# Performance work log

Hardware: AMD Instinct MI355X
Metric: run time of the kernel (lower is better)

## Reference

```python
import jax, jax.numpy as jnp
import numpy as np

B, I, J, DIM, H, DH = 2, 2048, 2048, 512, 8, 64
INNER = H * DH  # 512
SCALE = DH ** -0.5


def setup_inputs() -> dict:
    key = jax.random.key(0)
    ks = jax.random.split(key, 10)
    w = lambda k, shp: jax.random.normal(k, shp, dtype=jnp.float32) * 0.02
    return {
        "x": jax.random.normal(ks[0], (B, I, DIM), dtype=jnp.float32),
        "context": jax.random.normal(ks[1], (B, J, DIM), dtype=jnp.float32),
        "w_qk": w(ks[2], (DIM, INNER)),
        "w_cqk": w(ks[3], (DIM, INNER)),
        "w_v": w(ks[4], (DIM, INNER)),
        "w_cv": w(ks[5], (DIM, INNER)),
        "w_out": w(ks[6], (INNER, DIM)),
        "b_out": jnp.zeros((DIM,), dtype=jnp.float32),
        "w_cout": w(ks[7], (INNER, DIM)),
        "b_cout": jnp.zeros((DIM,), dtype=jnp.float32),
    }


def _split_heads(t):
    # [b, n, h*d] -> [b, h, n, d]
    b, n, _ = t.shape
    return t.reshape(b, n, H, DH).transpose(0, 2, 1, 3)


def reference(x, context, w_qk, w_cqk, w_v, w_cv, w_out, b_out, w_cout, b_cout):
    # projections (no bias, matching nn.Linear(..., bias=False))
    qk = _split_heads(x @ w_qk)            # [b,h,i,d]
    cqk = _split_heads(context @ w_cqk)    # [b,h,j,d]
    v = _split_heads(x @ w_v)              # [b,h,i,d]
    cv = _split_heads(context @ w_cv)      # [b,h,j,d]

    sim = jnp.einsum('bhid,bhjd->bhij', qk, cqk) * SCALE  # [b,h,i,j]

    attn = jax.nn.softmax(sim, axis=-1)        # row softmax over j
    context_attn = jax.nn.softmax(sim, axis=-2)  # column softmax over i

    out = jnp.einsum('bhij,bhjd->bhid', attn, cv)           # [b,h,i,d]
    context_out = jnp.einsum('bhji,bhjd->bhid', context_attn, v)  # [b,h,j_out=i? -> per einsum: i indexes last of attn]

    # merge heads: [b,h,n,d] -> [b,n,h*d]
    merge = lambda t: t.transpose(0, 2, 1, 3).reshape(t.shape[0], t.shape[2], INNER)
    out = merge(out) @ w_out + b_out                    # [b,i,dim]
    context_out = merge(context_out) @ w_cout + b_cout  # [b,j,dim]
    return (out, context_out)
```

## Files before the change

### kernel.cpp

```cpp
#include <hip/hip_runtime.h>

#define DEVI __device__ __forceinline__

typedef __attribute__((ext_vector_type(8))) short short8;
typedef __attribute__((ext_vector_type(4))) float f32x4;

struct alignas(8) us4 { unsigned short a, b, c, d; };

DEVI unsigned short f2bf(float f) {
    unsigned int u = __float_as_uint(f);
    u += 0x7fffU + ((u >> 16) & 1U);
    return (unsigned short)(u >> 16);
}

DEVI f32x4 mfma16(short8 a, short8 b, f32x4 c) {
    return __builtin_amdgcn_mfma_f32_16x16x32_bf16(a, b, c, 0, 0, 0);
}

DEVI unsigned pk2(float lo, float hi) {
    unsigned r0 = __float_as_uint(lo) + 0x8000u;
    unsigned r1 = __float_as_uint(hi) + 0x8000u;
    return __builtin_amdgcn_perm(r1, r0, 0x07060302u);
}

DEVI short8 mk8(unsigned a, unsigned b, unsigned c, unsigned d) {
    union { unsigned u[4]; short8 s; } x;
    x.u[0] = a; x.u[1] = b; x.u[2] = c; x.u[3] = d;
    return x.s;
}

#define GLDS(gp, sp) __builtin_amdgcn_global_load_lds( \
    (const __attribute__((address_space(1))) void*)(gp), \
    (__attribute__((address_space(3))) void*)(sp), 16, 0, 0)

#define VMCNT(n) asm volatile("s_waitcnt vmcnt(" #n ")" ::: "memory")
#define LGKMCNT0 asm volatile("s_waitcnt lgkmcnt(0)" ::: "memory")
#define MEMFENCE asm volatile("" ::: "memory")

#define SQC 0.42466089f

__global__ __launch_bounds__(256) void prep_kernel(
    const float* w0, const float* w1, const float* w2, const float* w3,
    const float* w4, const float* w5, short* __restrict__ wT)
{
    const float* srcs[6] = {w0, w1, w2, w3, w4, w5};
    int wz = blockIdx.x >> 6, rem = blockIdx.x & 63;
    const float* src = srcs[wz];
    short* dst = wT + (size_t)wz * 262144;
    int k0 = (rem >> 3) * 64, n0 = (rem & 7) * 64;
    __shared__ float tile[64][65];
    int t = threadIdx.x;
    int r = t >> 2, c0 = (t & 3) * 16;
#pragma unroll
    for (int ii = 0; ii < 4; ++ii) {
        float4 v = *(const float4*)(src + (size_t)(k0 + r) * 512 + n0 + c0 + ii * 4);
        tile[r][c0 + ii * 4 + 0] = v.x;
        tile[r][c0 + ii * 4 + 1] = v.y;
        tile[r][c0 + ii * 4 + 2] = v.z;
        tile[r][c0 + ii * 4 + 3] = v.w;
    }
    __syncthreads();
#pragma unroll
    for (int ii = 0; ii < 4; ++ii) {
        us4 o;
        o.a = f2bf(tile[c0 + ii * 4 + 0][r]);
        o.b = f2bf(tile[c0 + ii * 4 + 1][r]);
        o.c = f2bf(tile[c0 + ii * 4 + 2][r]);
        o.d = f2bf(tile[c0 + ii * 4 + 3][r]);
        *(us4*)(dst + (size_t)(n0 + r) * 512 + k0 + c0 + ii * 4) = o;
    }
}

__global__ __launch_bounds__(256, 4) void proj_kernel(
    const float* __restrict__ x, const float* __restrict__ ctx,
    const short* __restrict__ wT,
    short* __restrict__ QK, short* __restrict__ CQK,
    short* __restrict__ VT, short* __restrict__ CVT)
{
    __shared__ __align__(16) char smem[24576];
    short (*wst)[4096] = (short (*)[4096])smem;
    float (*ctile)[69] = (float (*)[69])smem;

    int p = blockIdx.z;
    const float* src = (p & 1) ? ctx : x;
    const short* wm = wT + (size_t)p * 262144;
    int wid = threadIdx.x >> 6, lane = threadIdx.x & 63, il = lane & 15, q = lane >> 4;
    int mb = blockIdx.x * 64, nb = blockIdx.y * 64;
    int srow = lane >> 3, scol8 = ((lane & 7) ^ srow) << 3;
    int key = il & 7;
    const short* wL0 = wm + (size_t)(nb + wid * 16 + srow) * 512 + scol8;
    const short* wL1 = wL0 + 8 * 512;
#define PSTAGE(s, ck) do { \
    GLDS(wL0 + (ck) * 64, &wst[s][wid * 1024]); \
    GLDS(wL1 + (ck) * 64, &wst[s][wid * 1024 + 512]); } while (0)

    PSTAGE(0, 0);
    PSTAGE(1, 1);

    const float* arow = src + (size_t)(mb + wid * 16 + il) * 512;
    short8 a[16];
#pragma unroll
    for (int j = 0; j < 16; ++j) {
        float4 f0 = *(const float4*)(arow + j * 32 + q * 8);
        float4 f1 = *(const float4*)(arow + j * 32 + q * 8 + 4);
        a[j] = mk8(pk2(f0.x, f0.y), pk2(f0.z, f0.w),
                   pk2(f1.x, f1.y), pk2(f1.z, f1.w));
    }

    f32x4 acc[4] = {};
    int sA = 0, sB = 1, sC = 2;
    for (int ck = 0; ck < 8; ++ck) {
        if (ck < 7) { VMCNT(2); } else { VMCNT(0); }
        MEMFENCE;
        __builtin_amdgcn_s_barrier();
        if (ck < 6) PSTAGE(sC, ck + 2);
#pragma unroll
        for (int kk = 0; kk < 2; ++kk) {
#pragma unroll
            for (int nj = 0; nj < 4; ++nj) {
                short8 b = *(const short8*)(&wst[sA][(nj * 16 + il) * 64 + ((((kk << 2) + q) ^ key) << 3)]);
                acc[nj] = mfma16(a[ck * 2 + kk], b, acc[nj]);
            }
        }
        int t_ = sA; sA = sB; sB = sC; sC = t_;
    }
#undef PSTAGE

    __syncthreads();
#pragma unroll
    for (int nj = 0; nj < 4; ++nj)
#pragma unroll
        for (int r = 0; r < 4; ++r)
            ctile[wid * 16 + q * 4 + r][nj * 16 + il] = acc[nj][r];
    __syncthreads();
    int t = threadIdx.x, row = t >> 2, seg = (t & 3) << 4;
    short tmp[16];
    int h = blockIdx.y;
    if (p < 2) {
        short* dst = p ? CQK : QK;
        int i = mb + row, b2 = i >> 11, iL = i & 2047;
#pragma unroll
        for (int e = 0; e < 16; ++e) tmp[e] = (short)f2bf(ctile[row][seg + e] * SQC);
        short* dp = dst + (((size_t)b2 * 8 + h) * 2048 + iL) * 64 + seg;
        *(short8*)dp = *(const short8*)tmp;
        *(short8*)(dp + 8) = *(const short8*)(tmp + 8);
    } else {
        short* dst = (p == 2) ? VT : CVT;
        int d = row;
        int i0 = mb + seg, b2 = i0 >> 11, iL = i0 & 2047;
#pragma unroll
        for (int e = 0; e < 16; ++e) tmp[e] = (short)f2bf(ctile[seg + e][d]);
        short* dp = dst + (((size_t)b2 * 8 + h) * 64 + d) * 2048 + iL;
        *(short8*)dp = *(const short8*)tmp;
        *(short8*)(dp + 8) = *(const short8*)(tmp + 8);
    }
}

__global__ __launch_bounds__(256, 3) void attn_kernel(
    const short* __restrict__ QK, const short* __restrict__ CQK,
    const short* __restrict__ VT, const short* __restrict__ CVT,
    short* __restrict__ OUTx, short* __restrict__ OUTc)
{
    __shared__ __align__(16) short Bt[3][4096];
    __shared__ __align__(16) short Wt[3][4096];

    int flat = blockIdx.x + (blockIdx.y << 4) + (blockIdx.z << 8);
    int bh = flat & 15;
    int ib = (flat >> 4) & 15;
    int z = flat >> 8;

    const short* Arows = z ? CQK : QK;
    const short* Bcols = z ? QK : CQK;
    const short* WTm   = z ? VT : CVT;
    short* Om          = z ? OUTc : OUTx;

    int b_ = bh >> 3, h = bh & 7;
    int w = threadIdx.x >> 6, lane = threadIdx.x & 63, il = lane & 15, q = lane >> 4;
    const short* Ab = Arows + (size_t)bh * 131072;
    const short* Bb = Bcols + (size_t)bh * 131072;
    const short* Wb = WTm + (size_t)bh * 131072;

    int srow = lane >> 3;
    int scol8 = ((lane & 7) ^ srow) << 3;
    int key = il & 7;

    int p0 = w * 16 + srow, p1 = p0 + 8;
    int j0p = (p0 & 0x23) | ((p0 & 0x0C) << 1) | ((p0 & 0x10) >> 2);
    int j1p = (p1 & 0x23) | ((p1 & 0x0C) << 1) | ((p1 & 0x10) >> 2);
    const short* BbL0 = Bb + j0p * 64 + scol8;
    const short* BbL1 = Bb + j1p * 64 + scol8;
    const short* WbL0 = Wb + (size_t)p0 * 2048 + scol8;
    const short* WbL1 = WbL0 + 8 * 2048;

#define STAGE(s, jt) do { \
    GLDS(BbL0 + (jt) * 4096, &Bt[s][w * 1024]); \
    GLDS(BbL1 + (jt) * 4096, &Bt[s][w * 1024 + 512]); \
    GLDS(WbL0 + (jt) * 64, &Wt[s][w * 1024]); \
    GLDS(WbL1 + (jt) * 64, &Wt[s][w * 1024 + 512]); } while (0)

    short* Areg = (w < 2) ? &Bt[2][0] : &Wt[2][0];
    int ar = (w & 1) * 2048;
    {
        const short* AbL = Ab + (size_t)(ib * 128 + w * 32 + srow) * 64 + scol8;
        GLDS(AbL, Areg + ar);
        GLDS(AbL + 512, Areg + ar + 512);
        GLDS(AbL + 1024, Areg + ar + 1024);
        GLDS(AbL + 1536, Areg + ar + 1536);
    }
    STAGE(0, 0);
    STAGE(1, 1);
    VMCNT(8);

    short8 aq[2][2];
#pragma unroll
    for (int rg = 0; rg < 2; ++rg) {
        const short* base = Areg + ((w & 1) * 32 + rg * 16 + il) * 64;
        aq[rg][0] = *(const short8*)(base + ((q ^ key) << 3));
        aq[rg][1] = *(const short8*)(base + (((q + 4) ^ key) << 3));
    }
    LGKMCNT0;
    __builtin_amdgcn_sched_barrier(0);

    f32x4 acc[2][4] = {};
    float s_acc[2] = {0.f, 0.f};

    int sA = 0, sB = 1, sC = 2;
    for (int jt = 0; jt < 32; ++jt) {
        if (jt < 31) { VMCNT(4); } else { VMCNT(0); }
        MEMFENCE;
        __builtin_amdgcn_s_barrier();
        if (jt < 30) STAGE(sC, jt + 2);

        short8 b0[4], b1[4];
#pragma unroll
        for (int nj = 0; nj < 4; ++nj) {
            const short* bb = &Bt[sA][(nj * 16 + il) * 64];
            b0[nj] = *(const short8*)(bb + ((q ^ key) << 3));
            b1[nj] = *(const short8*)(bb + (((q + 4) ^ key) << 3));
        }

        unsigned pw[2][8];
#pragma unroll
        for (int rg = 0; rg < 2; ++rg) {
#pragma unroll
            for (int nj = 0; nj < 4; ++nj) {
                f32x4 zz = {};
                zz = mfma16(b0[nj], aq[rg][0], zz);
                zz = mfma16(b1[nj], aq[rg][1], zz);
                float e0 = __builtin_amdgcn_exp2f(zz[0]);
                float e1 = __builtin_amdgcn_exp2f(zz[1]);
                float e2 = __builtin_amdgcn_exp2f(zz[2]);
                float e3 = __builtin_amdgcn_exp2f(zz[3]);
                s_acc[rg] += (e0 + e1) + (e2 + e3);
                pw[rg][nj * 2 + 0] = pk2(e0, e1);
                pw[rg][nj * 2 + 1] = pk2(e2, e3);
            }
        }
        short8 pa0[2] = { mk8(pw[0][0], pw[0][1], pw[0][2], pw[0][3]),
                          mk8(pw[1][0], pw[1][1], pw[1][2], pw[1][3]) };
        short8 pa1[2] = { mk8(pw[0][4], pw[0][5], pw[0][6], pw[0][7]),
                          mk8(pw[1][4], pw[1][5], pw[1][6], pw[1][7]) };

#pragma unroll
        for (int nd = 0; nd < 4; ++nd) {
            const short* vv = &Wt[sA][(nd * 16 + il) * 64];
            short8 v0 = *(const short8*)(vv + ((q ^ key) << 3));
            short8 v1 = *(const short8*)(vv + (((q + 4) ^ key) << 3));
#pragma unroll
            for (int rg = 0; rg < 2; ++rg) {
                acc[rg][nd] = mfma16(pa0[rg], v0, acc[rg][nd]);
                acc[rg][nd] = mfma16(pa1[rg], v1, acc[rg][nd]);
            }
        }
        int t_ = sA; sA = sB; sB = sC; sC = t_;
    }
#undef STAGE

    f32x4 inv[2];
#pragma unroll
    for (int rg = 0; rg < 2; ++rg) {
        float s = s_acc[rg];
        s += __shfl_xor(s, 16);
        s += __shfl_xor(s, 32);
#pragma unroll
        for (int r = 0; r < 4; ++r)
            inv[rg][r] = 1.0f / __shfl(s, q * 4 + r);
    }

#pragma unroll
    for (int rg = 0; rg < 2; ++rg) {
#pragma unroll
        for (int nd = 0; nd < 4; ++nd) {
#pragma unroll
            for (int r = 0; r < 4; ++r) {
                int i = ib * 128 + w * 32 + rg * 16 + q * 4 + r;
                Om[((size_t)b_ * 2048 + i) * 512 + h * 64 + nd * 16 + il] =
                    (short)f2bf(acc[rg][nd][r] * inv[rg][r]);
            }
        }
    }
}

__global__ __launch_bounds__(256, 4) void final_kernel(
    const short* __restrict__ OUTx, const short* __restrict__ OUTc,
    const short* __restrict__ wT,
    const float* __restrict__ b_out, const float* __restrict__ b_cout,
    float* __restrict__ dout)
{
    __shared__ __align__(16) short wst[3][4096];
    int z = blockIdx.z;
    const short* Am = z ? OUTc : OUTx;
    const short* wm = wT + (size_t)(4 + z) * 262144;
    const float* bias = z ? b_cout : b_out;
    float* D = dout + (size_t)z * 2097152;
    int wid = threadIdx.x >> 6, lane = threadIdx.x & 63, il = lane & 15, q = lane >> 4;
    int mb = blockIdx.x * 64, nb = blockIdx.y * 64;
    int srow = lane >> 3, scol8 = ((lane & 7) ^ srow) << 3;
    int key = il & 7;
    const short* wL0 = wm + (size_t)(nb + wid * 16 + srow) * 512 + scol8;
    const short* wL1 = wL0 + 8 * 512;
#define FSTAGE(s, ck) do { \
    GLDS(wL0 + (ck) * 64, &wst[s][wid * 1024]); \
    GLDS(wL1 + (ck) * 64, &wst[s][wid * 1024 + 512]); } while (0)

    FSTAGE(0, 0);
    FSTAGE(1, 1);
    const short* arow = Am + (size_t)(mb + wid * 16 + il) * 512;
    short8 a[16];
#pragma unroll
    for (int j = 0; j < 16; ++j) a[j] = *(const short8*)(arow + j * 32 + (q << 3));

    f32x4 acc[4] = {};
    int sA = 0, sB = 1, sC = 2;
    for (int ck = 0; ck < 8; ++ck) {
        if (ck < 7) { VMCNT(2); } else { VMCNT(0); }
        MEMFENCE;
        __builtin_amdgcn_s_barrier();
        if (ck < 6) FSTAGE(sC, ck + 2);
#pragma unroll
        for (int kk = 0; kk < 2; ++kk) {
#pragma unroll
            for (int nj = 0; nj < 4; ++nj) {
                short8 b = *(const short8*)(&wst[sA][(nj * 16 + il) * 64 + ((((kk << 2) + q) ^ key) << 3)]);
                acc[nj] = mfma16(a[ck * 2 + kk], b, acc[nj]);
            }
        }
        int t_ = sA; sA = sB; sB = sC; sC = t_;
    }
#undef FSTAGE

#pragma unroll
    for (int nj = 0; nj < 4; ++nj) {
        int c = nb + nj * 16 + il;
        float bi = bias[c];
#pragma unroll
        for (int r = 0; r < 4; ++r) {
            int m = mb + wid * 16 + q * 4 + r;
            D[(size_t)m * 512 + c] = acc[nj][r] + bi;
        }
    }
}

extern "C" void kernel_launch(void* const* d_in, const int* in_sizes, int n_in,
                              void* d_out, int out_size, void* d_ws, size_t ws_size,
                              hipStream_t stream)
{
    (void)in_sizes; (void)n_in; (void)out_size; (void)ws_size;
    const float* x      = (const float*)d_in[0];
    const float* ctx    = (const float*)d_in[1];
    const float* w_qk   = (const float*)d_in[2];
    const float* w_cqk  = (const float*)d_in[3];
    const float* w_v    = (const float*)d_in[4];
    const float* w_cv   = (const float*)d_in[5];
    const float* w_out  = (const float*)d_in[6];
    const float* b_out  = (const float*)d_in[7];
    const float* w_cout = (const float*)d_in[8];
    const float* b_cout = (const float*)d_in[9];
    float* dout = (float*)d_out;

    char* ws = (char*)d_ws;
    const size_t WSZ = (size_t)512 * 512 * 2;
    const size_t TSZ = (size_t)16 * 2048 * 64 * 2;
    short* wT   = (short*)ws;
    short* OUTx = (short*)(ws + 6 * WSZ);
    short* OUTc = (short*)(ws + 6 * WSZ + 1 * TSZ);
    short* QK   = (short*)(ws + 6 * WSZ + 2 * TSZ);
    short* CQK  = (short*)(ws + 6 * WSZ + 3 * TSZ);
    short* VT   = (short*)(ws + 6 * WSZ + 4 * TSZ);
    short* CVT  = (short*)(ws + 6 * WSZ + 5 * TSZ);

    prep_kernel<<<dim3(384), 256, 0, stream>>>(w_qk, w_cqk, w_v, w_cv, w_out, w_cout, wT);
    proj_kernel<<<dim3(64, 8, 4), 256, 0, stream>>>(x, ctx, wT, QK, CQK, VT, CVT);
    attn_kernel<<<dim3(16, 16, 2), 256, 0, stream>>>(QK, CQK, VT, CVT, OUTx, OUTc);
    final_kernel<<<dim3(64, 8, 2), 256, 0, stream>>>(OUTx, OUTc, wT, b_out, b_cout, dout);
}
```

Measured before the change: 176.9 us.

## Pre-convert activations to bf16 and use 128x128 LDS-tiled GEMMs for projections

The prep kernel now also converts x and context to bf16 buffers, so the projection GEMM no longer reads fp32 rows directly into registers. Projection and output GEMMs move from 64x64 tiles with 256 threads to 128x128 tiles with 512 threads. Both operands are staged through double-buffered LDS via global_load_lds, which raises per-block reuse of both A and B. The cost is an extra bf16 copy pass, fewer blocks per GEMM (512 and 256), and 64KB of LDS per block, which limits occupancy.

New measurement: 150.7 us. -14.8%, faster.

```diff
diff --git a/kernel.cpp b/kernel.cpp
--- a/kernel.cpp
+++ b/kernel.cpp
@@ -40,9 +40,22 @@
 #define SQC 0.42466089f
 
 __global__ __launch_bounds__(256) void prep_kernel(
+    const float* __restrict__ x, const float* __restrict__ ctx,
     const float* w0, const float* w1, const float* w2, const float* w3,
-    const float* w4, const float* w5, short* __restrict__ wT)
+    const float* w4, const float* w5,
+    short* __restrict__ Xb, short* __restrict__ Cb, short* __restrict__ wT)
 {
+    int z = blockIdx.z;
+    if (z < 2) {
+        const float* s = z ? ctx : x;
+        short* d = z ? Cb : Xb;
+        size_t t = (size_t)blockIdx.x * 256 + threadIdx.x;
+        float4 v = *(const float4*)(s + t * 4);
+        us4 o = { f2bf(v.x), f2bf(v.y), f2bf(v.z), f2bf(v.w) };
+        *(us4*)(d + t * 4) = o;
+        return;
+    }
+    if (blockIdx.x >= 384) return;
     const float* srcs[6] = {w0, w1, w2, w3, w4, w5};
     int wz = blockIdx.x >> 6, rem = blockIdx.x & 63;
     const float* src = srcs[wz];
@@ -71,88 +84,95 @@
     }
 }
 
-__global__ __launch_bounds__(256, 4) void proj_kernel(
-    const float* __restrict__ x, const float* __restrict__ ctx,
+__global__ __launch_bounds__(512, 2) void proj_kernel(
+    const short* __restrict__ Xb, const short* __restrict__ Cb,
     const short* __restrict__ wT,
     short* __restrict__ QK, short* __restrict__ CQK,
     short* __restrict__ VT, short* __restrict__ CVT)
 {
-    __shared__ __align__(16) char smem[24576];
-    short (*wst)[4096] = (short (*)[4096])smem;
-    float (*ctile)[69] = (float (*)[69])smem;
+    __shared__ __align__(16) char smem[65536];
+    float (*ctile)[65] = (float (*)[65])smem;
 
     int p = blockIdx.z;
-    const float* src = (p & 1) ? ctx : x;
+    const short* src = (p & 1) ? Cb : Xb;
     const short* wm = wT + (size_t)p * 262144;
-    int wid = threadIdx.x >> 6, lane = threadIdx.x & 63, il = lane & 15, q = lane >> 4;
-    int mb = blockIdx.x * 64, nb = blockIdx.y * 64;
+    int w = threadIdx.x >> 6, lane = threadIdx.x & 63, il = lane & 15, q = lane >> 4;
+    int wm_ = w & 3, wn = w >> 2;
+    int mb = blockIdx.x * 128, nb = blockIdx.y * 128;
     int srow = lane >> 3, scol8 = ((lane & 7) ^ srow) << 3;
     int key = il & 7;
-    const short* wL0 = wm + (size_t)(nb + wid * 16 + srow) * 512 + scol8;
-    const short* wL1 = wL0 + 8 * 512;
-#define PSTAGE(s, ck) do { \
-    GLDS(wL0 + (ck) * 64, &wst[s][wid * 1024]); \
-    GLDS(wL1 + (ck) * 64, &wst[s][wid * 1024 + 512]); } while (0)
+    const short* aL0 = src + (size_t)(mb + w * 16 + srow) * 512 + scol8;
+    const short* aL1 = aL0 + 8 * 512;
+    const short* bL0 = wm + (size_t)(nb + w * 16 + srow) * 512 + scol8;
+    const short* bL1 = bL0 + 8 * 512;
+#define TILE_A(buf) ((short*)smem + (buf) * 16384)
+#define TILE_B(buf) ((short*)smem + (buf) * 16384 + 8192)
+#define PSTAGE(buf, ck) do { \
+    GLDS(aL0 + (ck) * 64, TILE_A(buf) + w * 1024); \
+    GLDS(aL1 + (ck) * 64, TILE_A(buf) + w * 1024 + 512); \
+    GLDS(bL0 + (ck) * 64, TILE_B(buf) + w * 1024); \
+    GLDS(bL1 + (ck) * 64, TILE_B(buf) + w * 1024 + 512); } while (0)
 
     PSTAGE(0, 0);
-    PSTAGE(1, 1);
-
-    const float* arow = src + (size_t)(mb + wid * 16 + il) * 512;
-    short8 a[16];
-#pragma unroll
-    for (int j = 0; j < 16; ++j) {
-        float4 f0 = *(const float4*)(arow + j * 32 + q * 8);
-        float4 f1 = *(const float4*)(arow + j * 32 + q * 8 + 4);
-        a[j] = mk8(pk2(f0.x, f0.y), pk2(f0.z, f0.w),
-                   pk2(f1.x, f1.y), pk2(f1.z, f1.w));
-    }
-
-    f32x4 acc[4] = {};
-    int sA = 0, sB = 1, sC = 2;
+    f32x4 acc[2][4] = {};
+#pragma unroll
     for (int ck = 0; ck < 8; ++ck) {
-        if (ck < 7) { VMCNT(2); } else { VMCNT(0); }
+        int buf = ck & 1;
+        if (ck < 7) { PSTAGE(buf ^ 1, ck + 1); VMCNT(4); } else { VMCNT(0); }
+        __builtin_amdgcn_s_barrier();
+#pragma unroll
+        for (int kk = 0; kk < 2; ++kk) {
+            int ko = (((kk << 2) + q) ^ key) << 3;
+            short8 a0 = *(const short8*)(TILE_A(buf) + (wm_ * 32 + il) * 64 + ko);
+            short8 a1 = *(const short8*)(TILE_A(buf) + (wm_ * 32 + 16 + il) * 64 + ko);
+#pragma unroll
+            for (int nj = 0; nj < 4; ++nj) {
+                short8 b = *(const short8*)(TILE_B(buf) + (wn * 64 + nj * 16 + il) * 64 + ko);
+                acc[0][nj] = mfma16(a0, b, acc[0][nj]);
+                acc[1][nj] = mfma16(a1, b, acc[1][nj]);
+            }
+        }
         MEMFENCE;
         __builtin_amdgcn_s_barrier();
-        if (ck < 6) PSTAGE(sC, ck + 2);
-#pragma unroll
-        for (int kk = 0; kk < 2; ++kk) {
-#pragma unroll
-            for (int nj = 0; nj < 4; ++nj) {
-                short8 b = *(const short8*)(&wst[sA][(nj * 16 + il) * 64 + ((((kk << 2) + q) ^ key) << 3)]);
-                acc[nj] = mfma16(a[ck * 2 + kk], b, acc[nj]);
-            }
-        }
-        int t_ = sA; sA = sB; sB = sC; sC = t_;
     }
 #undef PSTAGE
 
-    __syncthreads();
-#pragma unroll
-    for (int nj = 0; nj < 4; ++nj)
-#pragma unroll
-        for (int r = 0; r < 4; ++r)
-            ctile[wid * 16 + q * 4 + r][nj * 16 + il] = acc[nj][r];
-    __syncthreads();
-    int t = threadIdx.x, row = t >> 2, seg = (t & 3) << 4;
-    short tmp[16];
-    int h = blockIdx.y;
-    if (p < 2) {
-        short* dst = p ? CQK : QK;
-        int i = mb + row, b2 = i >> 11, iL = i & 2047;
-#pragma unroll
-        for (int e = 0; e < 16; ++e) tmp[e] = (short)f2bf(ctile[row][seg + e] * SQC);
-        short* dp = dst + (((size_t)b2 * 8 + h) * 2048 + iL) * 64 + seg;
-        *(short8*)dp = *(const short8*)tmp;
-        *(short8*)(dp + 8) = *(const short8*)(tmp + 8);
-    } else {
-        short* dst = (p == 2) ? VT : CVT;
-        int d = row;
-        int i0 = mb + seg, b2 = i0 >> 11, iL = i0 & 2047;
-#pragma unroll
-        for (int e = 0; e < 16; ++e) tmp[e] = (short)f2bf(ctile[seg + e][d]);
-        short* dp = dst + (((size_t)b2 * 8 + h) * 64 + d) * 2048 + iL;
-        *(short8*)dp = *(const short8*)tmp;
-        *(short8*)(dp + 8) = *(const short8*)(tmp + 8);
+    int h0 = blockIdx.y * 2;
+#pragma unroll
+    for (int pass = 0; pass < 2; ++pass) {
+        __syncthreads();
+        if (wn == pass) {
+#pragma unroll
+            for (int mi = 0; mi < 2; ++mi)
+#pragma unroll
+                for (int nj = 0; nj < 4; ++nj)
+#pragma unroll
+                    for (int r = 0; r < 4; ++r)
+                        ctile[wm_ * 32 + mi * 16 + q * 4 + r][nj * 16 + il] = acc[mi][nj][r];
+        }
+        __syncthreads();
+        int t = threadIdx.x;
+        int h = h0 + pass;
+        short tmp[16];
+        if (p < 2) {
+            short* dst = p ? CQK : QK;
+            int row = t >> 2, seg = (t & 3) << 4;
+            int i = mb + row, b2 = i >> 11, iL = i & 2047;
+#pragma unroll
+            for (int e = 0; e < 16; ++e) tmp[e] = (short)f2bf(ctile[row][seg + e] * SQC);
+            short* dp = dst + (((size_t)b2 * 8 + h) * 2048 + iL) * 64 + seg;
+            *(short8*)dp = *(const short8*)tmp;
+            *(short8*)(dp + 8) = *(const short8*)(tmp + 8);
+        } else {
+            short* dst = (p == 2) ? VT : CVT;
+            int d = t >> 3, iseg = (t & 7) << 4;
+            int i0 = mb + iseg, b2 = i0 >> 11, iL = i0 & 2047;
+#pragma unroll
+            for (int e = 0; e < 16; ++e) tmp[e] = (short)f2bf(ctile[iseg + e][d]);
+            short* dp = dst + (((size_t)b2 * 8 + h) * 64 + d) * 2048 + iL;
+            *(short8*)dp = *(const short8*)tmp;
+            *(short8*)(dp + 8) = *(const short8*)(tmp + 8);
+        }
     }
 }
 
@@ -301,63 +321,68 @@
     }
 }
 
-__global__ __launch_bounds__(256, 4) void final_kernel(
+__global__ __launch_bounds__(512, 2) void final_kernel(
     const short* __restrict__ OUTx, const short* __restrict__ OUTc,
     const short* __restrict__ wT,
     const float* __restrict__ b_out, const float* __restrict__ b_cout,
     float* __restrict__ dout)
 {
-    __shared__ __align__(16) short wst[3][4096];
+    __shared__ __align__(16) char smem[65536];
     int z = blockIdx.z;
     const short* Am = z ? OUTc : OUTx;
     const short* wm = wT + (size_t)(4 + z) * 262144;
     const float* bias = z ? b_cout : b_out;
     float* D = dout + (size_t)z * 2097152;
-    int wid = threadIdx.x >> 6, lane = threadIdx.x & 63, il = lane & 15, q = lane >> 4;
-    int mb = blockIdx.x * 64, nb = blockIdx.y * 64;
+    int w = threadIdx.x >> 6, lane = threadIdx.x & 63, il = lane & 15, q = lane >> 4;
+    int wm_ = w & 3, wn = w >> 2;
+    int mb = blockIdx.x * 128, nb = blockIdx.y * 128;
     int srow = lane >> 3, scol8 = ((lane & 7) ^ srow) << 3;
     int key = il & 7;
-    const short* wL0 = wm + (size_t)(nb + wid * 16 + srow) * 512 + scol8;
-    const short* wL1 = wL0 + 8 * 512;
-#define FSTAGE(s, ck) do { \
-    GLDS(wL0 + (ck) * 64, &wst[s][wid * 1024]); \
-    GLDS(wL1 + (ck) * 64, &wst[s][wid * 1024 + 512]); } while (0)
+    const short* aL0 = Am + (size_t)(mb + w * 16 + srow) * 512 + scol8;
+    const short* aL1 = aL0 + 8 * 512;
+    const short* bL0 = wm + (size_t)(nb + w * 16 + srow) * 512 + scol8;
+    const short* bL1 = bL0 + 8 * 512;
+#define FSTAGE(buf, ck) do { \
+    GLDS(aL0 + (ck) * 64, TILE_A(buf) + w * 1024); \
+    GLDS(aL1 + (ck) * 64, TILE_A(buf) + w * 1024 + 512); \
+    GLDS(bL0 + (ck) * 64, TILE_B(buf) + w * 1024); \
+    GLDS(bL1 + (ck) * 64, TILE_B(buf) + w * 1024 + 512); } while (0)
 
     FSTAGE(0, 0);
-    FSTAGE(1, 1);
-    const short* arow = Am + (size_t)(mb + wid * 16 + il) * 512;
-    short8 a[16];
-#pragma unroll
-    for (int j = 0; j < 16; ++j) a[j] = *(const short8*)(arow + j * 32 + (q << 3));
-
-    f32x4 acc[4] = {};
-    int sA = 0, sB = 1, sC = 2;
+    f32x4 acc[2][4] = {};
+#pragma unroll
     for (int ck = 0; ck < 8; ++ck) {
-        if (ck < 7) { VMCNT(2); } else { VMCNT(0); }
+        int buf = ck & 1;
+        if (ck < 7) { FSTAGE(buf ^ 1, ck + 1); VMCNT(4); } else { VMCNT(0); }
+        __builtin_amdgcn_s_barrier();
+#pragma unroll
+        for (int kk = 0; kk < 2; ++kk) {
+            int ko = (((kk << 2) + q) ^ key) << 3;
+            short8 a0 = *(const short8*)(TILE_A(buf) + (wm_ * 32 + il) * 64 + ko);
+            short8 a1 = *(const short8*)(TILE_A(buf) + (wm_ * 32 + 16 + il) * 64 + ko);
+#pragma unroll
+            for (int nj = 0; nj < 4; ++nj) {
+                short8 b = *(const short8*)(TILE_B(buf) + (wn * 64 + nj * 16 + il) * 64 + ko);
+                acc[0][nj] = mfma16(a0, b, acc[0][nj]);
+                acc[1][nj] = mfma16(a1, b, acc[1][nj]);
+            }
+        }
         MEMFENCE;
         __builtin_amdgcn_s_barrier();
-        if (ck < 6) FSTAGE(sC, ck + 2);
-#pragma unroll
-        for (int kk = 0; kk < 2; ++kk) {
-#pragma unroll
-            for (int nj = 0; nj < 4; ++nj) {
-                short8 b = *(const short8*)(&wst[sA][(nj * 16 + il) * 64 + ((((kk << 2) + q) ^ key) << 3)]);
-                acc[nj] = mfma16(a[ck * 2 + kk], b, acc[nj]);
-            }
-        }
-        int t_ = sA; sA = sB; sB = sC; sC = t_;
     }
 #undef FSTAGE
 
 #pragma unroll
     for (int nj = 0; nj < 4; ++nj) {
-        int c = nb + nj * 16 + il;
+        int c = nb + wn * 64 + nj * 16 + il;
         float bi = bias[c];
 #pragma unroll
-        for (int r = 0; r < 4; ++r) {
-            int m = mb + wid * 16 + q * 4 + r;
-            D[(size_t)m * 512 + c] = acc[nj][r] + bi;
-        }
+        for (int mi = 0; mi < 2; ++mi)
+#pragma unroll
+            for (int r = 0; r < 4; ++r) {
+                int m = mb + wm_ * 32 + mi * 16 + q * 4 + r;
+                D[(size_t)m * 512 + c] = acc[mi][nj][r] + bi;
+            }
     }
 }
 
@@ -382,15 +407,18 @@
     const size_t WSZ = (size_t)512 * 512 * 2;
     const size_t TSZ = (size_t)16 * 2048 * 64 * 2;
     short* wT   = (short*)ws;
-    short* OUTx = (short*)(ws + 6 * WSZ);
-    short* OUTc = (short*)(ws + 6 * WSZ + 1 * TSZ);
+    short* Xb   = (short*)(ws + 6 * WSZ);
+    short* Cb   = (short*)(ws + 6 * WSZ + 1 * TSZ);
     short* QK   = (short*)(ws + 6 * WSZ + 2 * TSZ);
     short* CQK  = (short*)(ws + 6 * WSZ + 3 * TSZ);
     short* VT   = (short*)(ws + 6 * WSZ + 4 * TSZ);
     short* CVT  = (short*)(ws + 6 * WSZ + 5 * TSZ);
-
-    prep_kernel<<<dim3(384), 256, 0, stream>>>(w_qk, w_cqk, w_v, w_cv, w_out, w_cout, wT);
-    proj_kernel<<<dim3(64, 8, 4), 256, 0, stream>>>(x, ctx, wT, QK, CQK, VT, CVT);
+    short* OUTx = Xb;
+    short* OUTc = Cb;
+
+    prep_kernel<<<dim3(2048, 1, 3), 256, 0, stream>>>(
+        x, ctx, w_qk, w_cqk, w_v, w_cv, w_out, w_cout, Xb, Cb, wT);
+    proj_kernel<<<dim3(32, 4, 4), 512, 0, stream>>>(Xb, Cb, wT, QK, CQK, VT, CVT);
     attn_kernel<<<dim3(16, 16, 2), 256, 0, stream>>>(QK, CQK, VT, CVT, OUTx, OUTc);
-    final_kernel<<<dim3(64, 8, 2), 256, 0, stream>>>(OUTx, OUTc, wT, b_out, b_cout, dout);
-}
+    final_kernel<<<dim3(32, 4, 2), 512, 0, stream>>>(OUTx, OUTc, wT, b_out, b_cout, dout);
+}
```
